# Performance work log

Hardware: AMD Instinct MI355X
Metric: run time of the kernel (lower is better)

Reference implementation:

```python
import jax, jax.numpy as jnp
import numpy as np

D_MODEL = 2048
HEADS = 16


def setup_inputs() -> dict:
    key = jax.random.key(0)
    ks = jax.random.split(key, 9)
    s = 1.0 / np.sqrt(D_MODEL)
    x = jax.random.normal(ks[0], (2, 2048, D_MODEL), dtype=jnp.float32)
    wq = jax.random.uniform(ks[1], (D_MODEL, D_MODEL), jnp.float32, -s, s)
    wk = jax.random.uniform(ks[2], (D_MODEL, D_MODEL), jnp.float32, -s, s)
    wv = jax.random.uniform(ks[3], (D_MODEL, D_MODEL), jnp.float32, -s, s)
    wo = jax.random.uniform(ks[4], (D_MODEL, D_MODEL), jnp.float32, -s, s)
    bq = jax.random.uniform(ks[5], (D_MODEL,), jnp.float32, -s, s)
    bk = jax.random.uniform(ks[6], (D_MODEL,), jnp.float32, -s, s)
    bv = jax.random.uniform(ks[7], (D_MODEL,), jnp.float32, -s, s)
    bo = jax.random.uniform(ks[8], (D_MODEL,), jnp.float32, -s, s)
    return {"x": x, "wq": wq, "bq": bq, "wk": wk, "bk": bk,
            "wv": wv, "bv": bv, "wo": wo, "bo": bo}


def _split(t, heads):
    b, s, d = t.shape
    return t.reshape(b, s, heads, d // heads).transpose(0, 2, 1, 3)  # [b,h,s,dh]


def reference(x, wq, bq, wk, bk, wv, bv, wo, bo):
    q = x @ wq.T + bq
    k = x @ wk.T + bk
    v = x @ wv.T + bv
    q, k, v = _split(q, HEADS), _split(k, HEADS), _split(v, HEADS)
    dh = q.shape[-1]
    scale = 1.0 / np.sqrt(dh).astype(np.float32)
    score = jnp.einsum('bhqd,bhkd->bhqk', q, k) * scale  # [b,h,s,s]
    score = jax.nn.softmax(score.astype(jnp.float32), axis=-1).astype(q.dtype)
    out = jnp.einsum('bhqk,bhkd->bhqd', score, v)
    b, h, s, _ = out.shape
    out = out.transpose(0, 2, 1, 3).reshape(b, s, h * dh)
    return out @ wo.T + bo
```

## Files before the change

### kernel.cpp

```cpp
#include <hip/hip_runtime.h>
#include <cstdint>
#include <cstddef>

#define D_MODEL 2048
#define SEQ 2048
#define BATCH 2
#define HEADS 16
#define DH 128
#define MROWS (BATCH * SEQ)

typedef __attribute__((ext_vector_type(8))) short short8;
typedef __attribute__((ext_vector_type(4))) float f32x4;
typedef __attribute__((ext_vector_type(16))) float f32x16;
typedef __attribute__((ext_vector_type(2))) unsigned int uint2e;

__device__ __forceinline__ unsigned short f2bf(float f) {
    unsigned int u = __builtin_bit_cast(unsigned int, f);
    u += 0x7fffu + ((u >> 16) & 1u);
    return (unsigned short)(u >> 16);
}

__device__ __forceinline__ unsigned int cvt_pk_bf16(float lo, float hi) {
    unsigned int w;
    asm("v_cvt_pk_bf16_f32 %0, %1, %2" : "=v"(w) : "v"(lo), "v"(hi));
    return w;
}

__device__ __forceinline__ void swap32(unsigned int& x, unsigned int& y) {
#if __has_builtin(__builtin_amdgcn_permlane32_swap)
    uint2e r = __builtin_amdgcn_permlane32_swap(x, y, false, false);
    x = r[0]; y = r[1];
#else
    const int hi = (threadIdx.x >> 5) & 1;
    const unsigned int gx = (unsigned int)__shfl_xor((int)x, 32);
    const unsigned int gy = (unsigned int)__shfl_xor((int)y, 32);
    const unsigned int nx = hi ? gy : x;
    const unsigned int ny = hi ? y : gx;
    x = nx; y = ny;
#endif
}

__device__ __forceinline__ void gload_lds16(const unsigned short* g, unsigned short* l) {
    __builtin_amdgcn_global_load_lds(
        (const __attribute__((address_space(1))) void*)g,
        (__attribute__((address_space(3))) void*)l, 16, 0, 0);
}

__global__ __launch_bounds__(256) void cvt_kernel(const float* __restrict__ in,
                                                  unsigned short* __restrict__ out, int n4) {
    int i = blockIdx.x * 256 + threadIdx.x;
    if (i < n4) {
        const float4 v = reinterpret_cast<const float4*>(in)[i];
        ushort4 o;
        o.x = f2bf(v.x); o.y = f2bf(v.y); o.z = f2bf(v.z); o.w = f2bf(v.w);
        reinterpret_cast<ushort4*>(out)[i] = o;
    }
}

__global__ __launch_bounds__(256) void cvt4_kernel(const float* __restrict__ w0,
                                                   const float* __restrict__ w1,
                                                   const float* __restrict__ w2,
                                                   const float* __restrict__ w3,
                                                   unsigned short* __restrict__ out) {
    const int per = (D_MODEL * D_MODEL) / 4;
    int i = blockIdx.x * 256 + threadIdx.x;
    const int sel = i / per;
    const int off = i - sel * per;
    const float* s = sel == 0 ? w0 : sel == 1 ? w1 : sel == 2 ? w2 : w3;
    const float4 v = reinterpret_cast<const float4*>(s)[off];
    ushort4 o;
    o.x = f2bf(v.x); o.y = f2bf(v.y); o.z = f2bf(v.z); o.w = f2bf(v.w);
    reinterpret_cast<ushort4*>(out)[i] = o;
}

template <int MODE>
__global__ __launch_bounds__(512, 4)
void gemm8(const unsigned short* __restrict__ A,
           const unsigned short* __restrict__ W0,
           const unsigned short* __restrict__ W1,
           const unsigned short* __restrict__ W2,
           const float* __restrict__ b0f,
           const float* __restrict__ b1f,
           const float* __restrict__ b2f,
           unsigned short* __restrict__ O0,
           unsigned short* __restrict__ O1,
           unsigned short* __restrict__ O2,
           float* __restrict__ OF) {
    constexpr int BM = 256, BN = 128, BK = 32;
    constexpr int K = D_MODEL;
    constexpr int NTILES = K / BK;
    constexpr int NT_N = (MODE == 0 ? (3 * D_MODEL) / BN : D_MODEL / BN);
    __shared__ unsigned short As[2][BM * BK];
    __shared__ unsigned short Bs[2][BN * BK];

    const int tid  = threadIdx.x;
    const int lane = tid & 63;
    const int wid  = tid >> 6;

    constexpr int NWG = (MROWS / BM) * NT_N;
    const int wk = (blockIdx.x & 7) * (NWG >> 3) + (blockIdx.x >> 3);
    const int nt = wk % NT_N;
    const int mt = wk / NT_N;
    const int m0 = mt * BM;
    const int n0 = nt * BN;

    const unsigned short* Bw;
    const float* bias;
    int nloc;
    if constexpr (MODE == 0) {
        const int nsel = n0 >> 11;
        nloc = n0 & 2047;
        Bw = nsel == 0 ? W0 : (nsel == 1 ? W1 : W2);
        bias = nsel == 0 ? b0f : (nsel == 1 ? b1f : b2f);
    } else {
        Bw = W0; bias = b0f; nloc = n0;
    }

    const int srow = lane >> 2;
    const int schk = lane & 3;
    const int r0 = wid * 16 + srow;
    const int r1 = 128 + r0;
    const unsigned short* aSrc0 = A  + (size_t)(m0 + r0) * K + (schk ^ (r0 & 3)) * 8;
    const unsigned short* aSrc1 = A  + (size_t)(m0 + r1) * K + (schk ^ (r1 & 3)) * 8;
    const unsigned short* bSrc  = Bw + (size_t)(nloc + r0) * K + (schk ^ (r0 & 3)) * 8;

    const int fr = lane & 15, fg = lane >> 4;
    const int wm = wid >> 1, wn = wid & 1;
    const int ar = wm * 64 + fr;
    const int br = wn * 64 + fr;
    const int aoff = ar * BK + (fg ^ (ar & 3)) * 8;
    const int boff = br * BK + (fg ^ (br & 3)) * 8;

    f32x4 acc[4][4] = {};

#define STAGE(BUF, KOFF)                                                       \
    gload_lds16(aSrc0 + (KOFF), &As[BUF][(wid * 16) * BK]);                    \
    gload_lds16(aSrc1 + (KOFF), &As[BUF][(128 + wid * 16) * BK]);              \
    gload_lds16(bSrc + (KOFF), &Bs[BUF][(wid * 16) * BK]);

#define GBODY(T, BUF)                                                          \
    {                                                                          \
        if ((T) + 1 < NTILES) {                                                \
            asm volatile("s_waitcnt vmcnt(3)" ::: "memory");                   \
        } else {                                                               \
            asm volatile("s_waitcnt vmcnt(0)" ::: "memory");                   \
        }                                                                      \
        __builtin_amdgcn_s_barrier();                                          \
        asm volatile("" ::: "memory");                                         \
        short8 af[4], bf[4];                                                   \
        _Pragma("unroll")                                                      \
        for (int mi = 0; mi < 4; ++mi)                                         \
            af[mi] = *(const short8*)&As[BUF][aoff + mi * (16 * BK)];          \
        _Pragma("unroll")                                                      \
        for (int ni = 0; ni < 4; ++ni)                                         \
            bf[ni] = *(const short8*)&Bs[BUF][boff + ni * (16 * BK)];          \
        __builtin_amdgcn_s_setprio(1);                                         \
        _Pragma("unroll")                                                      \
        for (int mi = 0; mi < 4; ++mi)                                         \
            _Pragma("unroll")                                                  \
            for (int ni = 0; ni < 4; ++ni)                                     \
                acc[mi][ni] = __builtin_amdgcn_mfma_f32_16x16x32_bf16(         \
                    af[mi], bf[ni], acc[mi][ni], 0, 0, 0);                     \
        __builtin_amdgcn_s_setprio(0);                                         \
        asm volatile("s_waitcnt lgkmcnt(0)" ::: "memory");                     \
        __builtin_amdgcn_s_barrier();                                          \
        asm volatile("" ::: "memory");                                         \
        if ((T) + 2 < NTILES) { STAGE(BUF, ((T) + 2) * BK) }                   \
    }

    STAGE(0, 0)
    STAGE(1, BK)

    for (int t = 0; t < NTILES; t += 2) {
        GBODY(t, 0)
        GBODY(t + 1, 1)
    }
#undef GBODY
#undef STAGE

    if constexpr (MODE == 0) {
        const int nsel = n0 >> 11;
        if (nsel == 2) {
#pragma unroll
            for (int mi = 0; mi < 4; ++mi)
#pragma unroll
                for (int ni = 0; ni < 4; ++ni) {
                    const int col = nloc + wn * 64 + ni * 16 + fr;
                    const int row0 = m0 + wm * 64 + mi * 16 + fg * 4;
                    const float bv = bias[col];
                    ushort4 o4;
                    o4.x = f2bf(acc[mi][ni][0] + bv);
                    o4.y = f2bf(acc[mi][ni][1] + bv);
                    o4.z = f2bf(acc[mi][ni][2] + bv);
                    o4.w = f2bf(acc[mi][ni][3] + bv);
                    *(ushort4*)&O2[(size_t)col * MROWS + row0] = o4;
                }
        } else {
            unsigned short* Co = nsel ? O1 : O0;
#pragma unroll
            for (int mi = 0; mi < 4; ++mi)
#pragma unroll
                for (int ni = 0; ni < 4; ++ni) {
                    const int col = nloc + wn * 64 + ni * 16 + fr;
                    const float bv = bias[col];
#pragma unroll
                    for (int r = 0; r < 4; ++r) {
                        const int row = m0 + wm * 64 + mi * 16 + fg * 4 + r;
                        Co[(size_t)row * D_MODEL + col] = f2bf(acc[mi][ni][r] + bv);
                    }
                }
        }
    } else {
#pragma unroll
        for (int mi = 0; mi < 4; ++mi)
#pragma unroll
            for (int ni = 0; ni < 4; ++ni) {
                const int col = nloc + wn * 64 + ni * 16 + fr;
                const float bv = bias[col];
#pragma unroll
                for (int r = 0; r < 4; ++r) {
                    const int row = m0 + wm * 64 + mi * 16 + fg * 4 + r;
                    OF[(size_t)row * D_MODEL + col] = acc[mi][ni][r] + bv;
                }
            }
    }
}

__global__ __launch_bounds__(256, 2)
void flash_attn3(const unsigned short* __restrict__ Q, const unsigned short* __restrict__ Kg,
                 const unsigned short* __restrict__ VT, unsigned short* __restrict__ O) {
    constexpr int KVB = 64;
    constexpr int NT = SEQ / KVB;
    __shared__ unsigned short Ks[2 * KVB * DH];
    __shared__ unsigned short Vs[2 * DH * KVB];

    const int tid  = threadIdx.x;
    const int lane = tid & 63;
    const int wid  = tid >> 6;
    const int l31  = lane & 31;
    const int hi   = lane >> 5;

    const int qt = blockIdx.x & 15;
    const int bh = blockIdx.x >> 4;
    const int b = bh >> 4, h = bh & 15;
    const int qrow = qt * 128 + wid * 32 + l31;

    const unsigned short* Qp = Q + ((size_t)b * SEQ + qrow) * D_MODEL + h * DH;
    const unsigned short* Kp = Kg + (size_t)b * SEQ * D_MODEL + h * DH;
    const unsigned short* Vp = VT + (size_t)(h * DH) * MROWS + (size_t)b * SEQ;

    short8 qf[8];
#pragma unroll
    for (int kk = 0; kk < 8; ++kk)
        qf[kk] = *(const short8*)(Qp + kk * 16 + hi * 8);

    f32x16 acc[4] = {};
    float m_run = -1e30f, l_run = 0.f;
    const float Cc = 0.088388347648318447f * 1.4426950408889634f;
    const float THR = 8.0f / Cc;

    int co[8];
#pragma unroll
    for (int kk = 0; kk < 8; ++kk) co[kk] = ((kk * 2 + hi) ^ (l31 & 7)) * 8;

    int kroff[4], vroff[4];
#pragma unroll
    for (int q = 0; q < 4; ++q) {
        const int row_l = wid * 16 + q * 4 + (lane >> 4);
        kroff[q] = row_l * D_MODEL + ((lane & 15) ^ (row_l & 7)) * 8;
        const int d_l = wid * 32 + q * 8 + (lane >> 3);
        vroff[q] = d_l * MROWS + ((lane & 7) ^ (d_l & 7)) * 8;
    }
    unsigned short* KsW = Ks + (wid * 16) * DH;
    unsigned short* VsW = Vs + (wid * 32) * KVB;

#pragma unroll
    for (int q = 0; q < 4; ++q) {
        gload_lds16(Kp + kroff[q], KsW + q * 4 * DH);
        gload_lds16(Vp + vroff[q], VsW + q * 8 * KVB);
    }
    __syncthreads();

    for (int t = 0; t < NT; ++t) {
        const int cur = t & 1;
        if (t + 1 < NT) {
            const unsigned short* Kt = Kp + (size_t)((t + 1) * KVB) * D_MODEL;
            const unsigned short* Vt = Vp + (t + 1) * KVB;
            unsigned short* kd = KsW + (cur ^ 1) * (KVB * DH);
            unsigned short* vd = VsW + (cur ^ 1) * (DH * KVB);
#pragma unroll
            for (int q = 0; q < 4; ++q) {
                gload_lds16(Kt + kroff[q], kd + q * 4 * DH);
                gload_lds16(Vt + vroff[q], vd + q * 8 * KVB);
            }
        }
        const unsigned short* Kc = Ks + cur * (KVB * DH);
        const unsigned short* Vc = Vs + cur * (DH * KVB);

        f32x16 st0 = {}, st1 = {};
        __builtin_amdgcn_s_setprio(1);
#pragma unroll
        for (int kk = 0; kk < 8; ++kk) {
            const short8 kf0 = *(const short8*)&Kc[l31 * DH + co[kk]];
            const short8 kf1 = *(const short8*)&Kc[(32 + l31) * DH + co[kk]];
            st0 = __builtin_amdgcn_mfma_f32_32x32x16_bf16(kf0, qf[kk], st0, 0, 0, 0);
            st1 = __builtin_amdgcn_mfma_f32_32x32x16_bf16(kf1, qf[kk], st1, 0, 0, 0);
        }
        __builtin_amdgcn_s_setprio(0);

        float lm = -1e30f;
#pragma unroll
        for (int r = 0; r < 16; ++r) lm = fmaxf(lm, fmaxf(st0[r], st1[r]));
        {
            unsigned int a = __builtin_bit_cast(unsigned int, lm), bb = a;
            swap32(a, bb);
            lm = fmaxf(lm, __builtin_bit_cast(float, hi ? a : bb));
        }
        if (__any(lm > m_run + THR)) {
            const float mn = fmaxf(m_run, lm);
            const float sf = __builtin_amdgcn_exp2f((m_run - mn) * Cc);
            m_run = mn;
            l_run *= sf;
#pragma unroll
            for (int db = 0; db < 4; ++db)
#pragma unroll
                for (int r = 0; r < 16; ++r) acc[db][r] *= sf;
        }
        const float mc = m_run * Cc;
        float p0[16], p1[16];
        float ps = 0.f;
#pragma unroll
        for (int r = 0; r < 16; ++r) {
            p0[r] = __builtin_amdgcn_exp2f(__builtin_fmaf(st0[r], Cc, -mc));
            p1[r] = __builtin_amdgcn_exp2f(__builtin_fmaf(st1[r], Cc, -mc));
            ps += p0[r] + p1[r];
        }
        {
            unsigned int a = __builtin_bit_cast(unsigned int, ps), bb = a;
            swap32(a, bb);
            ps += __builtin_bit_cast(float, hi ? a : bb);
        }
        l_run += ps;

        unsigned int W0[8], W1[8];
#pragma unroll
        for (int tt = 0; tt < 8; ++tt) {
            W0[tt] = cvt_pk_bf16(p0[2 * tt], p0[2 * tt + 1]);
            W1[tt] = cvt_pk_bf16(p1[2 * tt], p1[2 * tt + 1]);
        }
        swap32(W0[0], W0[2]); swap32(W0[1], W0[3]);
        swap32(W0[4], W0[6]); swap32(W0[5], W0[7]);
        swap32(W1[0], W1[2]); swap32(W1[1], W1[3]);
        swap32(W1[4], W1[6]); swap32(W1[5], W1[7]);
        short8 pf[4];
        {
            uint4 f;
            f.x = W0[0]; f.y = W0[1]; f.z = W0[2]; f.w = W0[3];
            pf[0] = __builtin_bit_cast(short8, f);
            f.x = W0[4]; f.y = W0[5]; f.z = W0[6]; f.w = W0[7];
            pf[1] = __builtin_bit_cast(short8, f);
            f.x = W1[0]; f.y = W1[1]; f.z = W1[2]; f.w = W1[3];
            pf[2] = __builtin_bit_cast(short8, f);
            f.x = W1[4]; f.y = W1[5]; f.z = W1[6]; f.w = W1[7];
            pf[3] = __builtin_bit_cast(short8, f);
        }

        __builtin_amdgcn_s_setprio(1);
#pragma unroll
        for (int db = 0; db < 4; ++db) {
#pragma unroll
            for (int kk16 = 0; kk16 < 4; ++kk16) {
                const short8 vf = *(const short8*)&Vc[(db * 32 + l31) * KVB + co[kk16]];
                acc[db] = __builtin_amdgcn_mfma_f32_32x32x16_bf16(vf, pf[kk16], acc[db], 0, 0, 0);
            }
        }
        __builtin_amdgcn_s_setprio(0);
        __syncthreads();
    }

    const float inv_l = 1.0f / l_run;
    unsigned short* Op = O + ((size_t)b * SEQ + qrow) * D_MODEL + h * DH;
#pragma unroll
    for (int db = 0; db < 4; ++db)
#pragma unroll
        for (int g = 0; g < 4; ++g) {
            ushort4 o4;
            o4.x = f2bf(acc[db][4 * g + 0] * inv_l);
            o4.y = f2bf(acc[db][4 * g + 1] * inv_l);
            o4.z = f2bf(acc[db][4 * g + 2] * inv_l);
            o4.w = f2bf(acc[db][4 * g + 3] * inv_l);
            *(ushort4*)(Op + db * 32 + g * 8 + hi * 4) = o4;
        }
}

extern "C" void kernel_launch(void* const* d_in, const int* in_sizes, int n_in,
                              void* d_out, int out_size, void* d_ws, size_t ws_size,
                              hipStream_t stream) {
    (void)in_sizes; (void)n_in; (void)out_size; (void)ws_size;
    const float* x  = (const float*)d_in[0];
    const float* wq = (const float*)d_in[1];
    const float* bq = (const float*)d_in[2];
    const float* wk = (const float*)d_in[3];
    const float* bk = (const float*)d_in[4];
    const float* wv = (const float*)d_in[5];
    const float* bv = (const float*)d_in[6];
    const float* wo = (const float*)d_in[7];
    const float* bo = (const float*)d_in[8];
    float* out = (float*)d_out;

    unsigned short* ws = (unsigned short*)d_ws;
    const size_t NX = (size_t)MROWS * D_MODEL;
    const size_t NW = (size_t)D_MODEL * D_MODEL;
    unsigned short* xb  = ws;
    unsigned short* wqb = xb + NX;
    unsigned short* wkb = wqb + NW;
    unsigned short* wvb = wkb + NW;
    unsigned short* wob = wvb + NW;
    unsigned short* Qb  = wob + NW;
    unsigned short* Kb  = Qb + NX;
    unsigned short* VTb = Kb + NX;
    unsigned short* Ab  = VTb + NX;

    cvt_kernel<<<(unsigned)(NX / 1024), 256, 0, stream>>>(x, xb, (int)(NX / 4));
    cvt4_kernel<<<(unsigned)(4 * NW / 1024), 256, 0, stream>>>(wq, wk, wv, wo, wqb);

    gemm8<0><<<768, 512, 0, stream>>>(xb, wqb, wkb, wvb, bq, bk, bv,
                                      Qb, Kb, VTb, nullptr);

    flash_attn3<<<512, 256, 0, stream>>>(Qb, Kb, VTb, Ab);

    gemm8<1><<<256, 512, 0, stream>>>(Ab, wob, nullptr, nullptr, bo, nullptr, nullptr,
                                      nullptr, nullptr, nullptr, out);
}
```

Before: 297.7 us.

## Rework projection GEMM to BK=64 triple-buffered LDS pipeline with split MFMA phases

The projection GEMMs move from a double-buffered K=32 tile loop to a triple-buffered K=64 loop with an 8-way XOR swizzle. Global-to-LDS loads for tile t+2 are split across two compute halves, so memory traffic interleaves with the MFMAs. This halves the number of tile iterations and their barrier overhead. In exchange, LDS use grows to about 144KB per block and occupancy is lowered to 2 blocks per CU, with more barriers inside each iteration.

```diff
diff --git a/kernel.cpp b/kernel.cpp
--- a/kernel.cpp
+++ b/kernel.cpp
@@ -74,8 +74,8 @@
 }
 
 template <int MODE>
-__global__ __launch_bounds__(512, 4)
-void gemm8(const unsigned short* __restrict__ A,
+__global__ __launch_bounds__(512, 2)
+void gemmT(const unsigned short* __restrict__ A,
            const unsigned short* __restrict__ W0,
            const unsigned short* __restrict__ W1,
            const unsigned short* __restrict__ W2,
@@ -86,18 +86,20 @@
            unsigned short* __restrict__ O1,
            unsigned short* __restrict__ O2,
            float* __restrict__ OF) {
-    constexpr int BM = 256, BN = 128, BK = 32;
+    constexpr int BM = 256, BN = 128, BK = 64;
     constexpr int K = D_MODEL;
     constexpr int NTILES = K / BK;
-    constexpr int NT_N = (MODE == 0 ? (3 * D_MODEL) / BN : D_MODEL / BN);
-    __shared__ unsigned short As[2][BM * BK];
-    __shared__ unsigned short Bs[2][BN * BK];
+    constexpr int NT_N = (MODE == 0 ? 48 : 16);
+    constexpr int NWG = (MROWS / BM) * NT_N;
+    constexpr int ASZ = BM * BK;
+    constexpr int BSZ = BN * BK;
+    __shared__ unsigned short As[3][ASZ];
+    __shared__ unsigned short Bs[3][BSZ];
 
     const int tid  = threadIdx.x;
     const int lane = tid & 63;
     const int wid  = tid >> 6;
 
-    constexpr int NWG = (MROWS / BM) * NT_N;
     const int wk = (blockIdx.x & 7) * (NWG >> 3) + (blockIdx.x >> 3);
     const int nt = wk % NT_N;
     const int mt = wk / NT_N;
@@ -116,67 +118,99 @@
         Bw = W0; bias = b0f; nloc = n0;
     }
 
-    const int srow = lane >> 2;
-    const int schk = lane & 3;
-    const int r0 = wid * 16 + srow;
-    const int r1 = 128 + r0;
-    const unsigned short* aSrc0 = A  + (size_t)(m0 + r0) * K + (schk ^ (r0 & 3)) * 8;
-    const unsigned short* aSrc1 = A  + (size_t)(m0 + r1) * K + (schk ^ (r1 & 3)) * 8;
-    const unsigned short* bSrc  = Bw + (size_t)(nloc + r0) * K + (schk ^ (r0 & 3)) * 8;
+    const int srow = tid >> 3;
+    const int sch  = tid & 7;
+    const int ssw  = (sch ^ (srow & 7)) * 8;
+    const int sd   = srow * 64 + sch * 8;
+    const unsigned short* aS[4];
+#pragma unroll
+    for (int j = 0; j < 4; ++j) aS[j] = A + (size_t)(m0 + j * 64 + srow) * K + ssw;
+    const unsigned short* bS[2];
+#pragma unroll
+    for (int j = 0; j < 2; ++j) bS[j] = Bw + (size_t)(nloc + j * 64 + srow) * K + ssw;
 
     const int fr = lane & 15, fg = lane >> 4;
     const int wm = wid >> 1, wn = wid & 1;
-    const int ar = wm * 64 + fr;
-    const int br = wn * 64 + fr;
-    const int aoff = ar * BK + (fg ^ (ar & 3)) * 8;
-    const int boff = br * BK + (fg ^ (br & 3)) * 8;
+    int aoff[4][2], boff[4][2];
+#pragma unroll
+    for (int mi = 0; mi < 4; ++mi)
+#pragma unroll
+        for (int ks = 0; ks < 2; ++ks) {
+            aoff[mi][ks] = (wm * 64 + mi * 16 + fr) * BK + ((ks * 4 + fg) ^ (fr & 7)) * 8;
+            boff[mi][ks] = (wn * 64 + mi * 16 + fr) * BK + ((ks * 4 + fg) ^ (fr & 7)) * 8;
+        }
 
     f32x4 acc[4][4] = {};
 
-#define STAGE(BUF, KOFF)                                                       \
-    gload_lds16(aSrc0 + (KOFF), &As[BUF][(wid * 16) * BK]);                    \
-    gload_lds16(aSrc1 + (KOFF), &As[BUF][(128 + wid * 16) * BK]);              \
-    gload_lds16(bSrc + (KOFF), &Bs[BUF][(wid * 16) * BK]);
-
-#define GBODY(T, BUF)                                                          \
-    {                                                                          \
-        if ((T) + 1 < NTILES) {                                                \
-            asm volatile("s_waitcnt vmcnt(3)" ::: "memory");                   \
-        } else {                                                               \
-            asm volatile("s_waitcnt vmcnt(0)" ::: "memory");                   \
-        }                                                                      \
-        __builtin_amdgcn_s_barrier();                                          \
-        asm volatile("" ::: "memory");                                         \
-        short8 af[4], bf[4];                                                   \
-        _Pragma("unroll")                                                      \
-        for (int mi = 0; mi < 4; ++mi)                                         \
-            af[mi] = *(const short8*)&As[BUF][aoff + mi * (16 * BK)];          \
-        _Pragma("unroll")                                                      \
-        for (int ni = 0; ni < 4; ++ni)                                         \
-            bf[ni] = *(const short8*)&Bs[BUF][boff + ni * (16 * BK)];          \
-        __builtin_amdgcn_s_setprio(1);                                         \
-        _Pragma("unroll")                                                      \
-        for (int mi = 0; mi < 4; ++mi)                                         \
-            _Pragma("unroll")                                                  \
-            for (int ni = 0; ni < 4; ++ni)                                     \
-                acc[mi][ni] = __builtin_amdgcn_mfma_f32_16x16x32_bf16(         \
-                    af[mi], bf[ni], acc[mi][ni], 0, 0, 0);                     \
-        __builtin_amdgcn_s_setprio(0);                                         \
-        asm volatile("s_waitcnt lgkmcnt(0)" ::: "memory");                     \
-        __builtin_amdgcn_s_barrier();                                          \
-        asm volatile("" ::: "memory");                                         \
-        if ((T) + 2 < NTILES) { STAGE(BUF, ((T) + 2) * BK) }                   \
-    }
-
-    STAGE(0, 0)
-    STAGE(1, BK)
-
-    for (int t = 0; t < NTILES; t += 2) {
-        GBODY(t, 0)
-        GBODY(t + 1, 1)
-    }
-#undef GBODY
-#undef STAGE
+    unsigned short *pA0 = As[0], *pA1 = As[1], *pA2 = As[2];
+    unsigned short *pB0 = Bs[0], *pB1 = Bs[1], *pB2 = Bs[2];
+
+#define STG_A(P, T, J) gload_lds16(aS[J] + (T) * BK, (P) + (J) * 4096 + sd)
+#define STG_B(P, T, J) gload_lds16(bS[J] + (T) * BK, (P) + (J) * 4096 + sd)
+
+    STG_A(pA0, 0, 0); STG_A(pA0, 0, 1); STG_A(pA0, 0, 2); STG_A(pA0, 0, 3);
+    STG_B(pB0, 0, 0); STG_B(pB0, 0, 1);
+    STG_A(pA1, 1, 0); STG_A(pA1, 1, 1); STG_A(pA1, 1, 2); STG_A(pA1, 1, 3);
+    STG_B(pB1, 1, 0); STG_B(pB1, 1, 1);
+    asm volatile("s_waitcnt vmcnt(6)" ::: "memory");
+    __builtin_amdgcn_s_barrier();
+
+    for (int t = 0; t < NTILES; ++t) {
+        const bool more = (t + 2 < NTILES);
+        short8 aF[4][2], bF0[2][2];
+#pragma unroll
+        for (int mi = 0; mi < 4; ++mi)
+#pragma unroll
+            for (int ks = 0; ks < 2; ++ks)
+                aF[mi][ks] = *(const short8*)&pA0[aoff[mi][ks]];
+#pragma unroll
+        for (int ni = 0; ni < 2; ++ni)
+#pragma unroll
+            for (int ks = 0; ks < 2; ++ks)
+                bF0[ni][ks] = *(const short8*)&pB0[boff[ni][ks]];
+        if (more) { STG_A(pA2, t + 2, 0); STG_A(pA2, t + 2, 1); STG_B(pB2, t + 2, 0); }
+        __builtin_amdgcn_s_barrier();
+        asm volatile("s_waitcnt lgkmcnt(0)" ::: "memory");
+        __builtin_amdgcn_sched_barrier(0);
+        __builtin_amdgcn_s_setprio(1);
+#pragma unroll
+        for (int ks = 0; ks < 2; ++ks)
+#pragma unroll
+            for (int mi = 0; mi < 4; ++mi)
+#pragma unroll
+                for (int ni = 0; ni < 2; ++ni)
+                    acc[mi][ni] = __builtin_amdgcn_mfma_f32_16x16x32_bf16(
+                        aF[mi][ks], bF0[ni][ks], acc[mi][ni], 0, 0, 0);
+        __builtin_amdgcn_s_setprio(0);
+        __builtin_amdgcn_s_barrier();
+        short8 bF1[2][2];
+#pragma unroll
+        for (int ni = 0; ni < 2; ++ni)
+#pragma unroll
+            for (int ks = 0; ks < 2; ++ks)
+                bF1[ni][ks] = *(const short8*)&pB0[boff[2 + ni][ks]];
+        if (more) { STG_A(pA2, t + 2, 2); STG_A(pA2, t + 2, 3); STG_B(pB2, t + 2, 1); }
+        __builtin_amdgcn_s_barrier();
+        asm volatile("s_waitcnt lgkmcnt(0)" ::: "memory");
+        __builtin_amdgcn_sched_barrier(0);
+        __builtin_amdgcn_s_setprio(1);
+#pragma unroll
+        for (int ks = 0; ks < 2; ++ks)
+#pragma unroll
+            for (int mi = 0; mi < 4; ++mi)
+#pragma unroll
+                for (int ni = 0; ni < 2; ++ni)
+                    acc[mi][2 + ni] = __builtin_amdgcn_mfma_f32_16x16x32_bf16(
+                        aF[mi][ks], bF1[ni][ks], acc[mi][2 + ni], 0, 0, 0);
+        __builtin_amdgcn_s_setprio(0);
+        if (more) asm volatile("s_waitcnt vmcnt(6)" ::: "memory");
+        else      asm volatile("s_waitcnt vmcnt(0)" ::: "memory");
+        __builtin_amdgcn_s_barrier();
+        unsigned short* tA = pA0; pA0 = pA1; pA1 = pA2; pA2 = tA;
+        unsigned short* tB = pB0; pB0 = pB1; pB1 = pB2; pB2 = tB;
+    }
+#undef STG_A
+#undef STG_B
 
     if constexpr (MODE == 0) {
         const int nsel = n0 >> 11;
@@ -424,11 +458,11 @@
     cvt_kernel<<<(unsigned)(NX / 1024), 256, 0, stream>>>(x, xb, (int)(NX / 4));
     cvt4_kernel<<<(unsigned)(4 * NW / 1024), 256, 0, stream>>>(wq, wk, wv, wo, wqb);
 
-    gemm8<0><<<768, 512, 0, stream>>>(xb, wqb, wkb, wvb, bq, bk, bv,
+    gemmT<0><<<768, 512, 0, stream>>>(xb, wqb, wkb, wvb, bq, bk, bv,
                                       Qb, Kb, VTb, nullptr);
 
     flash_attn3<<<512, 256, 0, stream>>>(Qb, Kb, VTb, Ab);
 
-    gemm8<1><<<256, 512, 0, stream>>>(Ab, wob, nullptr, nullptr, bo, nullptr, nullptr,
+    gemmT<1><<<256, 512, 0, stream>>>(Ab, wob, nullptr, nullptr, bo, nullptr, nullptr,
                                       nullptr, nullptr, nullptr, out);
 }
```

Result: faster. 263.7 us (-11.4%).
